# Kernel optimization log

Hardware: AMD Instinct MI355X
Metric: run time of the kernel (lower is better)

Reference implementation:

```python
import jax, jax.numpy as jnp
import numpy as np

LN_EPS = 1e-5


def _layernorm(x, g, b):
    mu = x.mean(-1, keepdims=True)
    var = x.var(-1, keepdims=True)  # biased, matches torch LayerNorm
    return (x - mu) * jax.lax.rsqrt(var + LN_EPS) * g + b


def setup_inputs() -> dict:
    key = jax.random.key(0)
    ks = jax.random.split(key, 12)
    N, F, P, L, B, R, D = 100000, 128, 50000, 100, 1024, 5, 32
    return {
        "node_raw_features": jax.random.normal(ks[0], (N, F), jnp.float32),
        "retrieved_nodes": jax.random.randint(ks[1], (P, L), 0, N),
        "retrieved_indices": jax.random.randint(ks[2], (B, R), 0, P),
        "src_node_ids": jax.random.randint(ks[3], (B,), 0, N),
        "dst_node_ids": jax.random.randint(ks[4], (B,), 0, N),
        "node_interact_times": jax.random.uniform(ks[5], (B,), jnp.float32),
        "W_feat": jax.random.normal(ks[6], (F, D), jnp.float32) * 0.05,
        "b_feat": jnp.zeros((D,), jnp.float32),
        "w_struct": jax.random.normal(ks[7], (D,), jnp.float32) * 0.05,
        "b_struct": jnp.zeros((D,), jnp.float32),
        "ln_g": jnp.ones((D,), jnp.float32),
        "ln_b": jnp.zeros((D,), jnp.float32),
        "W_gcn": jax.random.normal(ks[8], (D, D), jnp.float32) * 0.05,
        "b_gcn": jnp.zeros((D,), jnp.float32),
        "W_out": jax.random.normal(ks[9], (D, D), jnp.float32) * 0.05,
        "b_out": jnp.zeros((D,), jnp.float32),
    }


def reference(node_raw_features, retrieved_nodes, retrieved_indices,
              src_node_ids, dst_node_ids, node_interact_times,
              W_feat, b_feat, w_struct, b_struct, ln_g, ln_b,
              W_gcn, b_gcn, W_out, b_out):
    # retrieval gathers
    demo_nodes = retrieved_nodes[retrieved_indices]            # [B,R,L]
    demo_raw = node_raw_features[demo_nodes]                   # [B,R,L,F]
    demo_feat = demo_raw @ W_feat + b_feat                     # [B,R,L,D]

    dst_raw = node_raw_features[dst_node_ids]                  # [B,F]
    cur_skill = dst_raw[:, 0].astype(jnp.int32)[:, None, None]
    demo_skill = demo_raw[..., 0].astype(jnp.int32)            # [B,R,L]
    sim = (demo_skill == cur_skill).astype(jnp.float32)[..., None]  # [B,R,L,1]
    fused = demo_feat + (sim * w_struct + b_struct)            # Linear(1,D) on sim

    hist = fused.mean(axis=1)                                  # [B,L,D]
    hist = _layernorm(hist, ln_g, ln_b)

    # per-sample chain graph: edge j->j+1 exists iff j+1 < num_valid
    valid = (demo_nodes[:, 0, :] > 0).sum(axis=1)              # [B]
    L = hist.shape[1]
    j = jnp.arange(L - 1)
    edge_mask = (j[None, :] + 1) < valid[:, None]              # [B,L-1]

    # GCN with self-loops: deg[v] = 1 + indegree(v)
    deg = 1.0 + jnp.pad(edge_mask.astype(hist.dtype), ((0, 0), (1, 0)))  # [B,L]
    xW = hist @ W_gcn                                          # [B,L,D]
    out = xW / deg[..., None]                                  # self-loop term 1/deg
    inv_norm = jax.lax.rsqrt(deg[:, :-1] * deg[:, 1:])         # [B,L-1]
    msg = jnp.where(edge_mask[..., None], xW[:, :-1] * inv_norm[..., None], 0.0)
    out = out + jnp.pad(msg, ((0, 0), (1, 0), (0, 0)))         # scatter to dst j+1
    gnn_out = jax.nn.relu(out + b_gcn)                         # [B,L,D]

    src_emb = gnn_out.mean(axis=1)                             # global_mean_pool
    dst_emb = dst_raw @ W_feat + b_feat

    src_emb = src_emb @ W_out + b_out
    dst_emb = dst_emb @ W_out + b_out
    # dropout is identity in eval mode
    return src_emb, dst_emb
```

## Files before the change

### kernel.cpp

```cpp
#include <hip/hip_runtime.h>

#define LN_EPS 1e-5f

static __device__ __forceinline__ float4 f4zero() { return make_float4(0.f, 0.f, 0.f, 0.f); }

__global__ __launch_bounds__(256) void k_feat(
    const float* __restrict__ X, const float* __restrict__ Wf,
    const float* __restrict__ bf, float* __restrict__ feat,
    int* __restrict__ skill, int N)
{
    __shared__ float Wl[128 * 32];
    for (int i = threadIdx.x; i < 128 * 32; i += 256) Wl[i] = Wf[i];
    __syncthreads();

    const int gid = blockIdx.x * 256 + threadIdx.x;
    const int row = gid >> 3;
    const int dg  = gid & 7;
    if (row >= N) return;

    const float4* __restrict__ X4 = (const float4*)X + (size_t)row * 32;
    const float4* __restrict__ W4 = (const float4*)Wl;

    float4 acc = *(const float4*)(bf + 4 * dg);

    #pragma unroll 8
    for (int f4 = 0; f4 < 32; ++f4) {
        const float4 xv = X4[f4];
        if (f4 == 0 && dg == 0) skill[row] = (int)xv.x;
        const float4 w0 = W4[(4 * f4 + 0) * 8 + dg];
        const float4 w1 = W4[(4 * f4 + 1) * 8 + dg];
        const float4 w2 = W4[(4 * f4 + 2) * 8 + dg];
        const float4 w3 = W4[(4 * f4 + 3) * 8 + dg];
        acc.x = fmaf(xv.x, w0.x, acc.x);
        acc.y = fmaf(xv.x, w0.y, acc.y);
        acc.z = fmaf(xv.x, w0.z, acc.z);
        acc.w = fmaf(xv.x, w0.w, acc.w);
        acc.x = fmaf(xv.y, w1.x, acc.x);
        acc.y = fmaf(xv.y, w1.y, acc.y);
        acc.z = fmaf(xv.y, w1.z, acc.z);
        acc.w = fmaf(xv.y, w1.w, acc.w);
        acc.x = fmaf(xv.z, w2.x, acc.x);
        acc.y = fmaf(xv.z, w2.y, acc.y);
        acc.z = fmaf(xv.z, w2.z, acc.z);
        acc.w = fmaf(xv.z, w2.w, acc.w);
        acc.x = fmaf(xv.w, w3.x, acc.x);
        acc.y = fmaf(xv.w, w3.y, acc.y);
        acc.z = fmaf(xv.w, w3.z, acc.z);
        acc.w = fmaf(xv.w, w3.w, acc.w);
    }

    *(float4*)(feat + (size_t)row * 32 + 4 * dg) = acc;
}

__global__ __launch_bounds__(128) void k_main(
    const float* __restrict__ feat, const int* __restrict__ skill,
    const int* __restrict__ rnodes, const int* __restrict__ ridx,
    const int* __restrict__ dst_ids,
    const float* __restrict__ w_struct, const float* __restrict__ b_struct,
    const float* __restrict__ ln_g, const float* __restrict__ ln_b,
    const float* __restrict__ Wg, const float* __restrict__ b_gcn,
    const float* __restrict__ Wo, const float* __restrict__ b_out,
    float* __restrict__ out, int B)
{
    __shared__ float Wgl[32 * 32];
    __shared__ float Wol[32 * 32];
    __shared__ float xwT[32][100];
    __shared__ float pooled[32];
    __shared__ int   pidx[5];
    __shared__ int   ivalid;
    __shared__ int   cskill;

    const int t = threadIdx.x, b = blockIdx.x;

    for (int i = t; i < 1024; i += 128) { Wgl[i] = Wg[i]; Wol[i] = Wo[i]; }
    if (t < 5)  pidx[t] = ridx[b * 5 + t];
    if (t == 5) ivalid = 0;
    if (t == 6) cskill = skill[dst_ids[b]];
    __syncthreads();

    const int l = t;
    float4 y[8];
    float4 xw[8];

    if (l < 100) {
        int nodes[5];
        #pragma unroll
        for (int r = 0; r < 5; ++r) nodes[r] = rnodes[(size_t)pidx[r] * 100 + l];
        if (nodes[0] > 0) atomicAdd(&ivalid, 1);

        int simc = 0;
        #pragma unroll
        for (int r = 0; r < 5; ++r) simc += (skill[nodes[r]] == cskill) ? 1 : 0;

        #pragma unroll
        for (int c = 0; c < 8; ++c) y[c] = f4zero();
        #pragma unroll
        for (int r = 0; r < 5; ++r) {
            const float4* fp = (const float4*)(feat + (size_t)nodes[r] * 32);
            #pragma unroll
            for (int c = 0; c < 8; ++c) {
                const float4 v = fp[c];
                y[c].x += v.x; y[c].y += v.y; y[c].z += v.z; y[c].w += v.w;
            }
        }

        const float simf = (float)simc * 0.2f;
        #pragma unroll
        for (int c = 0; c < 8; ++c) {
            const float4 ws = ((const float4*)w_struct)[c];
            const float4 bs = ((const float4*)b_struct)[c];
            y[c].x = fmaf(y[c].x, 0.2f, fmaf(simf, ws.x, bs.x));
            y[c].y = fmaf(y[c].y, 0.2f, fmaf(simf, ws.y, bs.y));
            y[c].z = fmaf(y[c].z, 0.2f, fmaf(simf, ws.z, bs.z));
            y[c].w = fmaf(y[c].w, 0.2f, fmaf(simf, ws.w, bs.w));
        }

        float mu = 0.f;
        #pragma unroll
        for (int c = 0; c < 8; ++c) mu += y[c].x + y[c].y + y[c].z + y[c].w;
        mu *= (1.f / 32.f);
        float var = 0.f;
        #pragma unroll
        for (int c = 0; c < 8; ++c) {
            float dx;
            dx = y[c].x - mu; var = fmaf(dx, dx, var);
            dx = y[c].y - mu; var = fmaf(dx, dx, var);
            dx = y[c].z - mu; var = fmaf(dx, dx, var);
            dx = y[c].w - mu; var = fmaf(dx, dx, var);
        }
        var *= (1.f / 32.f);
        const float rs = rsqrtf(var + LN_EPS);
        #pragma unroll
        for (int c = 0; c < 8; ++c) {
            const float4 g4 = ((const float4*)ln_g)[c];
            const float4 b4 = ((const float4*)ln_b)[c];
            y[c].x = fmaf((y[c].x - mu) * rs, g4.x, b4.x);
            y[c].y = fmaf((y[c].y - mu) * rs, g4.y, b4.y);
            y[c].z = fmaf((y[c].z - mu) * rs, g4.z, b4.z);
            y[c].w = fmaf((y[c].w - mu) * rs, g4.w, b4.w);
        }

        #pragma unroll
        for (int c = 0; c < 8; ++c) xw[c] = f4zero();
        #define XW_ACC(D, C) { \
            const float v = y[(D) / 4].C; \
            const float4* wr = (const float4*)(Wgl + (D) * 32); \
            _Pragma("unroll") \
            for (int c = 0; c < 8; ++c) { \
                const float4 w = wr[c]; \
                xw[c].x = fmaf(v, w.x, xw[c].x); \
                xw[c].y = fmaf(v, w.y, xw[c].y); \
                xw[c].z = fmaf(v, w.z, xw[c].z); \
                xw[c].w = fmaf(v, w.w, xw[c].w); } }
        #pragma unroll
        for (int q = 0; q < 8; ++q) {
            XW_ACC(4 * q + 0, x) XW_ACC(4 * q + 1, y)
            XW_ACC(4 * q + 2, z) XW_ACC(4 * q + 3, w)
        }
        #undef XW_ACC

        #pragma unroll
        for (int q = 0; q < 8; ++q) {
            xwT[4 * q + 0][l] = xw[q].x;
            xwT[4 * q + 1][l] = xw[q].y;
            xwT[4 * q + 2][l] = xw[q].z;
            xwT[4 * q + 3][l] = xw[q].w;
        }
    }
    __syncthreads();

    if (l < 100) {
        const int valid = ivalid;
        const bool hm = (l >= 1) && (l < valid);
        const float degl  = 1.f + ((l >= 1 && l < valid) ? 1.f : 0.f);
        const float deglm = 1.f + ((l - 1 >= 1 && (l - 1) < valid) ? 1.f : 0.f);
        const float invd  = 1.f / degl;
        const float invn  = hm ? rsqrtf(deglm * degl) : 0.f;
        const int lm = hm ? (l - 1) : l;
        #define GNN_D(D, C) { \
            const float m = hm ? xwT[D][lm] * invn : 0.f; \
            const float o = fmaf(xw[(D) / 4].C, invd, m) + bg4.C; \
            xw[(D) / 4].C = fmaxf(o, 0.f); }
        #pragma unroll
        for (int q = 0; q < 8; ++q) {
            const float4 bg4 = ((const float4*)b_gcn)[q];
            GNN_D(4 * q + 0, x) GNN_D(4 * q + 1, y)
            GNN_D(4 * q + 2, z) GNN_D(4 * q + 3, w)
        }
        #undef GNN_D
    }
    __syncthreads();

    if (l < 100) {
        #pragma unroll
        for (int q = 0; q < 8; ++q) {
            xwT[4 * q + 0][l] = xw[q].x;
            xwT[4 * q + 1][l] = xw[q].y;
            xwT[4 * q + 2][l] = xw[q].z;
            xwT[4 * q + 3][l] = xw[q].w;
        }
    }
    __syncthreads();

    if (t < 32) {
        float s = 0.f;
        for (int j = 0; j < 100; ++j) s += xwT[t][j];
        pooled[t] = s * 0.01f;
    }
    __syncthreads();

    if (t < 32) {
        float s = b_out[t];
        #pragma unroll 8
        for (int k = 0; k < 32; ++k) s = fmaf(pooled[k], Wol[k * 32 + t], s);
        out[(size_t)b * 32 + t] = s;
    } else if (t < 64) {
        const int d = t - 32;
        const float* fr = feat + (size_t)dst_ids[b] * 32;
        float s = b_out[d];
        #pragma unroll 8
        for (int k = 0; k < 32; ++k) s = fmaf(fr[k], Wol[k * 32 + d], s);
        out[(size_t)B * 32 + (size_t)b * 32 + d] = s;
    }
}

extern "C" void kernel_launch(void* const* d_in, const int* in_sizes, int n_in,
                              void* d_out, int out_size, void* d_ws, size_t ws_size,
                              hipStream_t stream)
{
    const float* X      = (const float*)d_in[0];
    const int*   rnodes = (const int*)  d_in[1];
    const int*   ridx   = (const int*)  d_in[2];
    const int*   dst    = (const int*)  d_in[4];
    const float* Wf  = (const float*)d_in[6];
    const float* bf  = (const float*)d_in[7];
    const float* wst = (const float*)d_in[8];
    const float* bst = (const float*)d_in[9];
    const float* lg  = (const float*)d_in[10];
    const float* lb  = (const float*)d_in[11];
    const float* Wg  = (const float*)d_in[12];
    const float* bg  = (const float*)d_in[13];
    const float* Wo  = (const float*)d_in[14];
    const float* bo  = (const float*)d_in[15];

    const int N = in_sizes[0] / 128;
    const int B = in_sizes[4];

    float* feat  = (float*)d_ws;
    int*   skill = (int*)((char*)d_ws + (size_t)N * 32 * sizeof(float));
    float* out   = (float*)d_out;

    k_feat<<<(N * 8 + 255) / 256, 256, 0, stream>>>(X, Wf, bf, feat, skill, N);
    k_main<<<B, 128, 0, stream>>>(feat, skill, rnodes, ridx, dst,
                                  wst, bst, lg, lb, Wg, bg, Wo, bo, out, B);
}
```

Measured before the change: 165.6 us.

## Split main kernel into row-parallel gather/LN/GCN-matmul and per-sample tail

The per-sample kernel, which used one thread per row with 100 of 128 threads active, is split in two. A new row kernel uses 8 threads per (b,l) row, each handling a float4 slice, so the feature gather is coalesced; layernorm uses shuffle reductions and the xW matmul reads Wg from shared memory. A tail kernel reads xW back from a workspace buffer, counts valid nodes with __syncthreads_count instead of a shared atomic, and does the GCN, pooling and output projection. This exposes more parallelism and coalesced loads, at the cost of an extra launch and a B*100*32 float round trip through global memory.

```diff
diff --git a/kernel.cpp b/kernel.cpp
--- a/kernel.cpp
+++ b/kernel.cpp
@@ -52,115 +52,125 @@
     *(float4*)(feat + (size_t)row * 32 + 4 * dg) = acc;
 }
 
-__global__ __launch_bounds__(128) void k_main(
+__global__ __launch_bounds__(256) void k_rows(
     const float* __restrict__ feat, const int* __restrict__ skill,
     const int* __restrict__ rnodes, const int* __restrict__ ridx,
     const int* __restrict__ dst_ids,
     const float* __restrict__ w_struct, const float* __restrict__ b_struct,
     const float* __restrict__ ln_g, const float* __restrict__ ln_b,
-    const float* __restrict__ Wg, const float* __restrict__ b_gcn,
+    const float* __restrict__ Wg, float* __restrict__ xw_out, int BL)
+{
+    __shared__ float Wgl[32 * 32];
+    for (int i = threadIdx.x; i < 1024; i += 256) Wgl[i] = Wg[i];
+    __syncthreads();
+
+    const int rid = blockIdx.x * 32 + (threadIdx.x >> 3);
+    if (rid >= BL) return;
+    const int dg   = threadIdx.x & 7;
+    const int lane = threadIdx.x & 63;
+    const int b = rid / 100;
+    const int l = rid - b * 100;
+
+    const int* __restrict__ rb = ridx + b * 5;
+    const int cskill = skill[dst_ids[b]];
+
+    float4 acc = f4zero();
+    int simc = 0;
+    #pragma unroll
+    for (int r = 0; r < 5; ++r) {
+        const int node = rnodes[(size_t)rb[r] * 100 + l];
+        simc += (skill[node] == cskill) ? 1 : 0;
+        const float4 v = *(const float4*)(feat + (size_t)node * 32 + 4 * dg);
+        acc.x += v.x; acc.y += v.y; acc.z += v.z; acc.w += v.w;
+    }
+
+    const float simf = (float)simc * 0.2f;
+    {
+        const float4 ws = ((const float4*)w_struct)[dg];
+        const float4 bs = ((const float4*)b_struct)[dg];
+        acc.x = fmaf(acc.x, 0.2f, fmaf(simf, ws.x, bs.x));
+        acc.y = fmaf(acc.y, 0.2f, fmaf(simf, ws.y, bs.y));
+        acc.z = fmaf(acc.z, 0.2f, fmaf(simf, ws.z, bs.z));
+        acc.w = fmaf(acc.w, 0.2f, fmaf(simf, ws.w, bs.w));
+    }
+
+    float part = acc.x + acc.y + acc.z + acc.w;
+    part += __shfl_xor(part, 1);
+    part += __shfl_xor(part, 2);
+    part += __shfl_xor(part, 4);
+    const float mu = part * (1.f / 32.f);
+    float dx, sq;
+    dx = acc.x - mu; sq  = dx * dx;
+    dx = acc.y - mu; sq  = fmaf(dx, dx, sq);
+    dx = acc.z - mu; sq  = fmaf(dx, dx, sq);
+    dx = acc.w - mu; sq  = fmaf(dx, dx, sq);
+    sq += __shfl_xor(sq, 1);
+    sq += __shfl_xor(sq, 2);
+    sq += __shfl_xor(sq, 4);
+    const float rs = rsqrtf(sq * (1.f / 32.f) + LN_EPS);
+
+    float4 y;
+    {
+        const float4 g4 = ((const float4*)ln_g)[dg];
+        const float4 b4 = ((const float4*)ln_b)[dg];
+        y.x = fmaf((acc.x - mu) * rs, g4.x, b4.x);
+        y.y = fmaf((acc.y - mu) * rs, g4.y, b4.y);
+        y.z = fmaf((acc.z - mu) * rs, g4.z, b4.z);
+        y.w = fmaf((acc.w - mu) * rs, g4.w, b4.w);
+    }
+
+    float h[32];
+    const int base = lane & ~7;
+    #pragma unroll
+    for (int s = 0; s < 8; ++s) {
+        h[4 * s + 0] = __shfl(y.x, base + s, 64);
+        h[4 * s + 1] = __shfl(y.y, base + s, 64);
+        h[4 * s + 2] = __shfl(y.z, base + s, 64);
+        h[4 * s + 3] = __shfl(y.w, base + s, 64);
+    }
+
+    float4 o = f4zero();
+    const float4* __restrict__ W4 = (const float4*)Wgl;
+    #pragma unroll
+    for (int k = 0; k < 32; ++k) {
+        const float4 w = W4[k * 8 + dg];
+        o.x = fmaf(h[k], w.x, o.x);
+        o.y = fmaf(h[k], w.y, o.y);
+        o.z = fmaf(h[k], w.z, o.z);
+        o.w = fmaf(h[k], w.w, o.w);
+    }
+
+    *(float4*)(xw_out + (size_t)rid * 32 + 4 * dg) = o;
+}
+
+__global__ __launch_bounds__(128) void k_tail(
+    const float* __restrict__ feat, const int* __restrict__ rnodes,
+    const int* __restrict__ ridx, const int* __restrict__ dst_ids,
+    const float* __restrict__ xw_in, const float* __restrict__ b_gcn,
     const float* __restrict__ Wo, const float* __restrict__ b_out,
     float* __restrict__ out, int B)
 {
-    __shared__ float Wgl[32 * 32];
     __shared__ float Wol[32 * 32];
     __shared__ float xwT[32][100];
     __shared__ float pooled[32];
-    __shared__ int   pidx[5];
-    __shared__ int   ivalid;
-    __shared__ int   cskill;
+    __shared__ int   pidx0;
 
     const int t = threadIdx.x, b = blockIdx.x;
 
-    for (int i = t; i < 1024; i += 128) { Wgl[i] = Wg[i]; Wol[i] = Wo[i]; }
-    if (t < 5)  pidx[t] = ridx[b * 5 + t];
-    if (t == 5) ivalid = 0;
-    if (t == 6) cskill = skill[dst_ids[b]];
+    for (int i = t; i < 1024; i += 128) Wol[i] = Wo[i];
+    if (t == 0) pidx0 = ridx[b * 5];
     __syncthreads();
 
     const int l = t;
-    float4 y[8];
+    const int node0 = (l < 100) ? rnodes[(size_t)pidx0 * 100 + l] : 0;
+    const int valid = __syncthreads_count(node0 > 0);
+
     float4 xw[8];
-
     if (l < 100) {
-        int nodes[5];
-        #pragma unroll
-        for (int r = 0; r < 5; ++r) nodes[r] = rnodes[(size_t)pidx[r] * 100 + l];
-        if (nodes[0] > 0) atomicAdd(&ivalid, 1);
-
-        int simc = 0;
-        #pragma unroll
-        for (int r = 0; r < 5; ++r) simc += (skill[nodes[r]] == cskill) ? 1 : 0;
-
-        #pragma unroll
-        for (int c = 0; c < 8; ++c) y[c] = f4zero();
-        #pragma unroll
-        for (int r = 0; r < 5; ++r) {
-            const float4* fp = (const float4*)(feat + (size_t)nodes[r] * 32);
-            #pragma unroll
-            for (int c = 0; c < 8; ++c) {
-                const float4 v = fp[c];
-                y[c].x += v.x; y[c].y += v.y; y[c].z += v.z; y[c].w += v.w;
-            }
-        }
-
-        const float simf = (float)simc * 0.2f;
-        #pragma unroll
-        for (int c = 0; c < 8; ++c) {
-            const float4 ws = ((const float4*)w_struct)[c];
-            const float4 bs = ((const float4*)b_struct)[c];
-            y[c].x = fmaf(y[c].x, 0.2f, fmaf(simf, ws.x, bs.x));
-            y[c].y = fmaf(y[c].y, 0.2f, fmaf(simf, ws.y, bs.y));
-            y[c].z = fmaf(y[c].z, 0.2f, fmaf(simf, ws.z, bs.z));
-            y[c].w = fmaf(y[c].w, 0.2f, fmaf(simf, ws.w, bs.w));
-        }
-
-        float mu = 0.f;
-        #pragma unroll
-        for (int c = 0; c < 8; ++c) mu += y[c].x + y[c].y + y[c].z + y[c].w;
-        mu *= (1.f / 32.f);
-        float var = 0.f;
-        #pragma unroll
-        for (int c = 0; c < 8; ++c) {
-            float dx;
-            dx = y[c].x - mu; var = fmaf(dx, dx, var);
-            dx = y[c].y - mu; var = fmaf(dx, dx, var);
-            dx = y[c].z - mu; var = fmaf(dx, dx, var);
-            dx = y[c].w - mu; var = fmaf(dx, dx, var);
-        }
-        var *= (1.f / 32.f);
-        const float rs = rsqrtf(var + LN_EPS);
-        #pragma unroll
-        for (int c = 0; c < 8; ++c) {
-            const float4 g4 = ((const float4*)ln_g)[c];
-            const float4 b4 = ((const float4*)ln_b)[c];
-            y[c].x = fmaf((y[c].x - mu) * rs, g4.x, b4.x);
-            y[c].y = fmaf((y[c].y - mu) * rs, g4.y, b4.y);
-            y[c].z = fmaf((y[c].z - mu) * rs, g4.z, b4.z);
-            y[c].w = fmaf((y[c].w - mu) * rs, g4.w, b4.w);
-        }
-
-        #pragma unroll
-        for (int c = 0; c < 8; ++c) xw[c] = f4zero();
-        #define XW_ACC(D, C) { \
-            const float v = y[(D) / 4].C; \
-            const float4* wr = (const float4*)(Wgl + (D) * 32); \
-            _Pragma("unroll") \
-            for (int c = 0; c < 8; ++c) { \
-                const float4 w = wr[c]; \
-                xw[c].x = fmaf(v, w.x, xw[c].x); \
-                xw[c].y = fmaf(v, w.y, xw[c].y); \
-                xw[c].z = fmaf(v, w.z, xw[c].z); \
-                xw[c].w = fmaf(v, w.w, xw[c].w); } }
+        const float4* xp = (const float4*)(xw_in + ((size_t)b * 100 + l) * 32);
         #pragma unroll
         for (int q = 0; q < 8; ++q) {
-            XW_ACC(4 * q + 0, x) XW_ACC(4 * q + 1, y)
-            XW_ACC(4 * q + 2, z) XW_ACC(4 * q + 3, w)
-        }
-        #undef XW_ACC
-
-        #pragma unroll
-        for (int q = 0; q < 8; ++q) {
+            xw[q] = xp[q];
             xwT[4 * q + 0][l] = xw[q].x;
             xwT[4 * q + 1][l] = xw[q].y;
             xwT[4 * q + 2][l] = xw[q].z;
@@ -170,7 +180,6 @@
     __syncthreads();
 
     if (l < 100) {
-        const int valid = ivalid;
         const bool hm = (l >= 1) && (l < valid);
         const float degl  = 1.f + ((l >= 1 && l < valid) ? 1.f : 0.f);
         const float deglm = 1.f + ((l - 1 >= 1 && (l - 1) < valid) ? 1.f : 0.f);
@@ -245,12 +254,17 @@
 
     const int N = in_sizes[0] / 128;
     const int B = in_sizes[4];
+    const int BL = B * 100;
 
     float* feat  = (float*)d_ws;
     int*   skill = (int*)((char*)d_ws + (size_t)N * 32 * sizeof(float));
+    size_t skill_bytes = (((size_t)N * sizeof(int)) + 15) & ~(size_t)15;
+    float* xw_ws = (float*)((char*)skill + skill_bytes);
     float* out   = (float*)d_out;
 
     k_feat<<<(N * 8 + 255) / 256, 256, 0, stream>>>(X, Wf, bf, feat, skill, N);
-    k_main<<<B, 128, 0, stream>>>(feat, skill, rnodes, ridx, dst,
-                                  wst, bst, lg, lb, Wg, bg, Wo, bo, out, B);
-}
+    k_rows<<<(BL * 8 + 255) / 256, 256, 0, stream>>>(feat, skill, rnodes, ridx, dst,
+                                                     wst, bst, lg, lb, Wg, xw_ws, BL);
+    k_tail<<<B, 128, 0, stream>>>(feat, rnodes, ridx, dst, xw_ws,
+                                  bg, Wo, bo, out, B);
+}
```

Result: faster. 161.5 us (-2.5%).
